# Kernel optimization log

Hardware: AMD Instinct MI355X
Metric: run time of the kernel (lower is better)

The kernel has to match this reference:

```python
import jax, jax.numpy as jnp
import numpy as np

B, S, I, H = 16, 2048, 1024, 1024

def setup_inputs() -> dict:
    key = jax.random.key(0)
    ks = jax.random.split(key, 6)
    scale_ih = 1.0 / np.sqrt(I)
    scale_hh = 1.0 / np.sqrt(H)
    return {
        "x": jax.random.normal(ks[0], (B, S, I), dtype=jnp.float32),
        "hx": jax.random.normal(ks[1], (B, H), dtype=jnp.float32),
        "W_ih": jax.random.normal(ks[2], (H, I), dtype=jnp.float32) * scale_ih,
        "W_hh": jax.random.normal(ks[3], (H, H), dtype=jnp.float32) * scale_hh,
        "b_ih": jax.random.normal(ks[4], (H,), dtype=jnp.float32) * scale_ih,
        "b_hh": jax.random.normal(ks[5], (H,), dtype=jnp.float32) * scale_hh,
    }

def reference(x, hx, W_ih, W_hh, b_ih, b_hh):
    # Faithful to RecurrentCellWrapper: the Python loop passes the SAME
    # initial hx to the cell at every timestep (hx is never updated),
    # so all steps are independent and fully vectorizable.
    # cell: h' = tanh(x_t @ W_ih^T + b_ih + hx @ W_hh^T + b_hh)
    h_term = hx @ W_hh.T + b_hh + b_ih            # [B, H], shared across steps
    x_term = jnp.einsum('bsi,hi->bsh', x, W_ih)   # [B, S, H]
    out = jnp.tanh(x_term + h_term[:, None, :])   # [B, S, H]
    # batch_first=True: output already [batch, seq, hidden]
    return out
```

## Files before the change

kernel.cpp:

```cpp
#include <hip/hip_runtime.h>
#include <hip/hip_bf16.h>
#include <stdint.h>


#define M_TOT 32768
#define N_TOT 1024
#define K_TOT 1024

typedef short short8 __attribute__((ext_vector_type(8)));
typedef float f32x4  __attribute__((ext_vector_type(4)));

#define WS_XBF_OFF   0
#define WS_WBF_OFF   67108864
#define WS_HT_OFF    69206016

__device__ __forceinline__ unsigned short f32_to_bf16_rne(float f) {
    union { float f; unsigned int u; } v; v.f = f;
    unsigned int u = v.u;
    unsigned int r = u + 0x7fffu + ((u >> 16) & 1u);
    return (unsigned short)(r >> 16);
}

__device__ __forceinline__ float fast_tanh(float z) {
    float e = __expf(2.0f * z);
    return 1.0f - 2.0f / (e + 1.0f);
}

__global__ void convert_kernel(const float* __restrict__ x,
                               const float* __restrict__ wih,
                               unsigned short* __restrict__ xbf,
                               unsigned short* __restrict__ wbf) {
    const int NXV = 33554432 / 8;
    const int NWV = 1048576 / 8;
    int stride = gridDim.x * blockDim.x;
    for (int v = blockIdx.x * blockDim.x + threadIdx.x; v < NXV + NWV; v += stride) {
        const float* src; unsigned short* dst; long long base;
        if (v < NXV) { src = x;   dst = xbf; base = (long long)v * 8; }
        else         { src = wih; dst = wbf; base = (long long)(v - NXV) * 8; }
        float4 a = *(const float4*)(src + base);
        float4 b = *(const float4*)(src + base + 4);
        union { unsigned short s[8]; uint4 u; } o;
        o.s[0] = f32_to_bf16_rne(a.x); o.s[1] = f32_to_bf16_rne(a.y);
        o.s[2] = f32_to_bf16_rne(a.z); o.s[3] = f32_to_bf16_rne(a.w);
        o.s[4] = f32_to_bf16_rne(b.x); o.s[5] = f32_to_bf16_rne(b.y);
        o.s[6] = f32_to_bf16_rne(b.z); o.s[7] = f32_to_bf16_rne(b.w);
        *(uint4*)(dst + base) = o.u;
    }
}

__global__ void hterm_kernel(const float* __restrict__ hx,
                             const float* __restrict__ whh,
                             const float* __restrict__ bih,
                             const float* __restrict__ bhh,
                             float* __restrict__ ht) {
    int lane = threadIdx.x & 63;
    int w    = threadIdx.x >> 6;
    int wg   = blockIdx.x * 4 + w;
    int b = wg >> 10, h = wg & 1023;
    const float* hr = hx  + (long long)b * 1024;
    const float* wr = whh + (long long)h * 1024;
    float s = 0.f;
#pragma unroll
    for (int p = 0; p < 4; ++p) {
        int idx = p * 256 + lane * 4;
        float4 a = *(const float4*)(hr + idx);
        float4 c = *(const float4*)(wr + idx);
        s += a.x * c.x + a.y * c.y + a.z * c.z + a.w * c.w;
    }
#pragma unroll
    for (int d = 32; d > 0; d >>= 1) s += __shfl_down(s, d, 64);
    if (lane == 0) ht[wg] = s + bih[h] + bhh[h];
}

#define GLDS16(gp, lp) \
    __builtin_amdgcn_global_load_lds((const __attribute__((address_space(1))) void*)(gp), \
                                     (__attribute__((address_space(3))) void*)(lp), 16, 0, 0)

__global__ __launch_bounds__(256) void gemm_tanh_kernel(
    const unsigned short* __restrict__ A,
    const unsigned short* __restrict__ Bm,
    const float* __restrict__ ht,
    float* __restrict__ out)
{
    __shared__ __align__(16) char lds[16384];

    const int tid = threadIdx.x;
    const int w = tid >> 6, l = tid & 63;
    const int bid = blockIdx.x;
    const int tile_n = bid & 7;
    const int tile_m = bid >> 3;
    const int m0 = tile_m << 7, n0 = tile_n << 7;

    const int r0 = (w * 2 + 0) * 16 + (l >> 2);
    const int r1 = (w * 2 + 1) * 16 + (l >> 2);
    const int slot = l & 3;
    const int qg0 = (slot - (r0 >> 1)) & 3;
    const int qg1 = (slot - (r1 >> 1)) & 3;
    const unsigned short* gA0 = A  + (long long)(m0 + r0) * K_TOT + qg0 * 8;
    const unsigned short* gA1 = A  + (long long)(m0 + r1) * K_TOT + qg1 * 8;
    const unsigned short* gB0 = Bm + (long long)(n0 + r0) * K_TOT + qg0 * 8;
    const unsigned short* gB1 = Bm + (long long)(n0 + r1) * K_TOT + qg1 * 8;
    char* ldsA0 = lds + (w * 2 + 0) * 1024;
    char* ldsA1 = lds + (w * 2 + 1) * 1024;
    char* ldsB0 = lds + 8192 + (w * 2 + 0) * 1024;
    char* ldsB1 = lds + 8192 + (w * 2 + 1) * 1024;

    const int wm = w & 1, wn = w >> 1;
    const int lm = l & 15, q = l >> 4;
    int offA[4], offB[4];
#pragma unroll
    for (int t = 0; t < 4; ++t) {
        int rr = wm * 64 + t * 16 + lm;
        offA[t] = rr * 64 + (((q + (rr >> 1)) & 3) << 4);
        int nn = wn * 64 + t * 16 + lm;
        offB[t] = 8192 + nn * 64 + (((q + (nn >> 1)) & 3) << 4);
    }

    f32x4 acc[4][4];
#pragma unroll
    for (int i = 0; i < 4; ++i)
#pragma unroll
        for (int j = 0; j < 4; ++j)
            acc[i][j] = (f32x4){0.f, 0.f, 0.f, 0.f};

    for (int k0 = 0; k0 < K_TOT; k0 += 32) {
        GLDS16(gA0 + k0, ldsA0);
        GLDS16(gA1 + k0, ldsA1);
        GLDS16(gB0 + k0, ldsB0);
        GLDS16(gB1 + k0, ldsB1);
        __syncthreads();

        short8 af[4], bf[4];
#pragma unroll
        for (int t = 0; t < 4; ++t) {
            af[t] = *(const short8*)(lds + offA[t]);
            bf[t] = *(const short8*)(lds + offB[t]);
        }
#pragma unroll
        for (int mt = 0; mt < 4; ++mt)
#pragma unroll
            for (int nt = 0; nt < 4; ++nt)
                acc[mt][nt] = __builtin_amdgcn_mfma_f32_16x16x32_bf16(
                    af[mt], bf[nt], acc[mt][nt], 0, 0, 0);
        __syncthreads();
    }

    const int b = tile_m >> 4;
    float htv[4];
#pragma unroll
    for (int nt = 0; nt < 4; ++nt)
        htv[nt] = ht[b * 1024 + n0 + wn * 64 + nt * 16 + lm];

#pragma unroll
    for (int mt = 0; mt < 4; ++mt) {
#pragma unroll
        for (int nt = 0; nt < 4; ++nt) {
            int n = n0 + wn * 64 + nt * 16 + lm;
#pragma unroll
            for (int r = 0; r < 4; ++r) {
                int m = m0 + wm * 64 + mt * 16 + q * 4 + r;
                float z = acc[mt][nt][r] + htv[nt];
                out[(long long)m * N_TOT + n] = fast_tanh(z);
            }
        }
    }
}

extern "C" void kernel_launch(void* const* d_in, const int* in_sizes, int n_in,
                              void* d_out, int out_size, void* d_ws, size_t ws_size,
                              hipStream_t stream) {
    const float* x    = (const float*)d_in[0];
    const float* hx   = (const float*)d_in[1];
    const float* wih  = (const float*)d_in[2];
    const float* whh  = (const float*)d_in[3];
    const float* bih  = (const float*)d_in[4];
    const float* bhh  = (const float*)d_in[5];
    float* out = (float*)d_out;

    unsigned short* xbf = (unsigned short*)((char*)d_ws + WS_XBF_OFF);
    unsigned short* wbf = (unsigned short*)((char*)d_ws + WS_WBF_OFF);
    float*          htp = (float*)((char*)d_ws + WS_HT_OFF);

    hterm_kernel<<<4096, 256, 0, stream>>>(hx, whh, bih, bhh, htp);
    convert_kernel<<<2048, 256, 0, stream>>>(x, wih, xbf, wbf);
    gemm_tanh_kernel<<<2048, 256, 0, stream>>>(xbf, wbf, htp, out);
}
```

Measured before the change: 344.8 us.

## Fuse x bf16 conversion into GEMM A-tile load and merge prep kernels

Removes the separate pass that converts x to bf16 in workspace. The GEMM now loads fp32 x directly, rounds it to bf16 in registers and writes it to LDS in the same swizzled layout. The h-term and W_ih conversion kernels are merged into one launch, and the block-to-tile mapping is remapped so that co-resident blocks share B tiles and A rows. This saves one full 128MB read and 64MB write/read round trip of x, at the cost of heavier synchronous global loads inside the GEMM loop instead of async LDS loads.

```diff
diff --git a/kernel.cpp b/kernel.cpp
--- a/kernel.cpp
+++ b/kernel.cpp
@@ -1,5 +1,4 @@
 #include <hip/hip_runtime.h>
-#include <hip/hip_bf16.h>
 #include <stdint.h>
 
 
@@ -10,15 +9,15 @@
 typedef short short8 __attribute__((ext_vector_type(8)));
 typedef float f32x4  __attribute__((ext_vector_type(4)));
 
-#define WS_XBF_OFF   0
-#define WS_WBF_OFF   67108864
-#define WS_HT_OFF    69206016
+#define WS_WBF_OFF 0
+#define WS_HT_OFF  2097152
 
-__device__ __forceinline__ unsigned short f32_to_bf16_rne(float f) {
-    union { float f; unsigned int u; } v; v.f = f;
-    unsigned int u = v.u;
-    unsigned int r = u + 0x7fffu + ((u >> 16) & 1u);
-    return (unsigned short)(r >> 16);
+__device__ __forceinline__ unsigned int pack2_bf16_rne(float lo, float hi) {
+    unsigned int a = __float_as_uint(lo);
+    unsigned int b = __float_as_uint(hi);
+    a = (a + 0x7fffu + ((a >> 16) & 1u)) >> 16;
+    b = (b + 0x7fffu + ((b >> 16) & 1u)) & 0xffff0000u;
+    return a | b;
 }
 
 __device__ __forceinline__ float fast_tanh(float z) {
@@ -26,50 +25,43 @@
     return 1.0f - 2.0f / (e + 1.0f);
 }
 
-__global__ void convert_kernel(const float* __restrict__ x,
-                               const float* __restrict__ wih,
-                               unsigned short* __restrict__ xbf,
-                               unsigned short* __restrict__ wbf) {
-    const int NXV = 33554432 / 8;
-    const int NWV = 1048576 / 8;
-    int stride = gridDim.x * blockDim.x;
-    for (int v = blockIdx.x * blockDim.x + threadIdx.x; v < NXV + NWV; v += stride) {
-        const float* src; unsigned short* dst; long long base;
-        if (v < NXV) { src = x;   dst = xbf; base = (long long)v * 8; }
-        else         { src = wih; dst = wbf; base = (long long)(v - NXV) * 8; }
-        float4 a = *(const float4*)(src + base);
-        float4 b = *(const float4*)(src + base + 4);
-        union { unsigned short s[8]; uint4 u; } o;
-        o.s[0] = f32_to_bf16_rne(a.x); o.s[1] = f32_to_bf16_rne(a.y);
-        o.s[2] = f32_to_bf16_rne(a.z); o.s[3] = f32_to_bf16_rne(a.w);
-        o.s[4] = f32_to_bf16_rne(b.x); o.s[5] = f32_to_bf16_rne(b.y);
-        o.s[6] = f32_to_bf16_rne(b.z); o.s[7] = f32_to_bf16_rne(b.w);
-        *(uint4*)(dst + base) = o.u;
+__global__ void prep_kernel(const float* __restrict__ hx,
+                            const float* __restrict__ whh,
+                            const float* __restrict__ bih,
+                            const float* __restrict__ bhh,
+                            const float* __restrict__ wih,
+                            unsigned short* __restrict__ wbf,
+                            float* __restrict__ ht) {
+    int bid = blockIdx.x;
+    if (bid < 4096) {
+        int lane = threadIdx.x & 63;
+        int w    = threadIdx.x >> 6;
+        int wg   = bid * 4 + w;
+        int b = wg >> 10, h = wg & 1023;
+        const float* hr = hx  + (long long)b * 1024;
+        const float* wr = whh + (long long)h * 1024;
+        float s = 0.f;
+#pragma unroll
+        for (int p = 0; p < 4; ++p) {
+            int idx = p * 256 + lane * 4;
+            float4 a = *(const float4*)(hr + idx);
+            float4 c = *(const float4*)(wr + idx);
+            s += a.x * c.x + a.y * c.y + a.z * c.z + a.w * c.w;
+        }
+#pragma unroll
+        for (int d = 32; d > 0; d >>= 1) s += __shfl_down(s, d, 64);
+        if (lane == 0) ht[wg] = s + bih[h] + bhh[h];
+    } else {
+        long long base = ((long long)(bid - 4096) * 256 + threadIdx.x) * 8;
+        float4 a = *(const float4*)(wih + base);
+        float4 b = *(const float4*)(wih + base + 4);
+        uint4 o;
+        o.x = pack2_bf16_rne(a.x, a.y);
+        o.y = pack2_bf16_rne(a.z, a.w);
+        o.z = pack2_bf16_rne(b.x, b.y);
+        o.w = pack2_bf16_rne(b.z, b.w);
+        *(uint4*)(wbf + base) = o;
     }
-}
-
-__global__ void hterm_kernel(const float* __restrict__ hx,
-                             const float* __restrict__ whh,
-                             const float* __restrict__ bih,
-                             const float* __restrict__ bhh,
-                             float* __restrict__ ht) {
-    int lane = threadIdx.x & 63;
-    int w    = threadIdx.x >> 6;
-    int wg   = blockIdx.x * 4 + w;
-    int b = wg >> 10, h = wg & 1023;
-    const float* hr = hx  + (long long)b * 1024;
-    const float* wr = whh + (long long)h * 1024;
-    float s = 0.f;
-#pragma unroll
-    for (int p = 0; p < 4; ++p) {
-        int idx = p * 256 + lane * 4;
-        float4 a = *(const float4*)(hr + idx);
-        float4 c = *(const float4*)(wr + idx);
-        s += a.x * c.x + a.y * c.y + a.z * c.z + a.w * c.w;
-    }
-#pragma unroll
-    for (int d = 32; d > 0; d >>= 1) s += __shfl_down(s, d, 64);
-    if (lane == 0) ht[wg] = s + bih[h] + bhh[h];
 }
 
 #define GLDS16(gp, lp) \
@@ -77,7 +69,7 @@
                                      (__attribute__((address_space(3))) void*)(lp), 16, 0, 0)
 
 __global__ __launch_bounds__(256) void gemm_tanh_kernel(
-    const unsigned short* __restrict__ A,
+    const float* __restrict__ X,
     const unsigned short* __restrict__ Bm,
     const float* __restrict__ ht,
     float* __restrict__ out)
@@ -86,9 +78,12 @@
 
     const int tid = threadIdx.x;
     const int w = tid >> 6, l = tid & 63;
+
     const int bid = blockIdx.x;
-    const int tile_n = bid & 7;
-    const int tile_m = bid >> 3;
+    const int x = bid & 7;
+    const int tile_n = (bid >> 3) & 7;
+    const int g = bid >> 6;
+    const int tile_m = x * 32 + g;
     const int m0 = tile_m << 7, n0 = tile_n << 7;
 
     const int r0 = (w * 2 + 0) * 16 + (l >> 2);
@@ -96,14 +91,20 @@
     const int slot = l & 3;
     const int qg0 = (slot - (r0 >> 1)) & 3;
     const int qg1 = (slot - (r1 >> 1)) & 3;
-    const unsigned short* gA0 = A  + (long long)(m0 + r0) * K_TOT + qg0 * 8;
-    const unsigned short* gA1 = A  + (long long)(m0 + r1) * K_TOT + qg1 * 8;
     const unsigned short* gB0 = Bm + (long long)(n0 + r0) * K_TOT + qg0 * 8;
     const unsigned short* gB1 = Bm + (long long)(n0 + r1) * K_TOT + qg1 * 8;
-    char* ldsA0 = lds + (w * 2 + 0) * 1024;
-    char* ldsA1 = lds + (w * 2 + 1) * 1024;
     char* ldsB0 = lds + 8192 + (w * 2 + 0) * 1024;
     char* ldsB1 = lds + 8192 + (w * 2 + 1) * 1024;
+
+    const int rowA0 = tid >> 2;
+    const int rowA1 = rowA0 + 64;
+    const int sA = tid & 3;
+    const int qgA0 = (sA - (rowA0 >> 1)) & 3;
+    const int qgA1 = (sA - (rowA1 >> 1)) & 3;
+    const float* gAf0 = X + (long long)(m0 + rowA0) * K_TOT + qgA0 * 8;
+    const float* gAf1 = X + (long long)(m0 + rowA1) * K_TOT + qgA1 * 8;
+    const int ldsAoff0 = rowA0 * 64 + sA * 16;
+    const int ldsAoff1 = rowA1 * 64 + sA * 16;
 
     const int wm = w & 1, wn = w >> 1;
     const int lm = l & 15, q = l >> 4;
@@ -124,10 +125,23 @@
             acc[i][j] = (f32x4){0.f, 0.f, 0.f, 0.f};
 
     for (int k0 = 0; k0 < K_TOT; k0 += 32) {
-        GLDS16(gA0 + k0, ldsA0);
-        GLDS16(gA1 + k0, ldsA1);
         GLDS16(gB0 + k0, ldsB0);
         GLDS16(gB1 + k0, ldsB1);
+        float4 a00 = *(const float4*)(gAf0 + k0);
+        float4 a01 = *(const float4*)(gAf0 + k0 + 4);
+        float4 a10 = *(const float4*)(gAf1 + k0);
+        float4 a11 = *(const float4*)(gAf1 + k0 + 4);
+        uint4 w0, w1;
+        w0.x = pack2_bf16_rne(a00.x, a00.y);
+        w0.y = pack2_bf16_rne(a00.z, a00.w);
+        w0.z = pack2_bf16_rne(a01.x, a01.y);
+        w0.w = pack2_bf16_rne(a01.z, a01.w);
+        w1.x = pack2_bf16_rne(a10.x, a10.y);
+        w1.y = pack2_bf16_rne(a10.z, a10.w);
+        w1.z = pack2_bf16_rne(a11.x, a11.y);
+        w1.w = pack2_bf16_rne(a11.z, a11.w);
+        *(uint4*)(lds + ldsAoff0) = w0;
+        *(uint4*)(lds + ldsAoff1) = w1;
         __syncthreads();
 
         short8 af[4], bf[4];
@@ -177,11 +191,9 @@
     const float* bhh  = (const float*)d_in[5];
     float* out = (float*)d_out;
 
-    unsigned short* xbf = (unsigned short*)((char*)d_ws + WS_XBF_OFF);
     unsigned short* wbf = (unsigned short*)((char*)d_ws + WS_WBF_OFF);
     float*          htp = (float*)((char*)d_ws + WS_HT_OFF);
 
-    hterm_kernel<<<4096, 256, 0, stream>>>(hx, whh, bih, bhh, htp);
-    convert_kernel<<<2048, 256, 0, stream>>>(x, wih, xbf, wbf);
-    gemm_tanh_kernel<<<2048, 256, 0, stream>>>(xbf, wbf, htp, out);
+    prep_kernel<<<4608, 256, 0, stream>>>(hx, whh, bih, bhh, wih, wbf, htp);
+    gemm_tanh_kernel<<<2048, 256, 0, stream>>>(x, wbf, htp, out);
 }
```

Result: slower. 361.9 us (+5.0%).
